# Kernel optimization log

Measured on AMD Instinct MI355X. Metric: run time of the kernel, lower is better.

The kernel has to match this reference:

```python
import jax, jax.numpy as jnp
import numpy as np

B, S, E, H, WIN = 1, 2048, 1024, 16, 256
D = E // H  # head_out = 64


def setup_inputs() -> dict:
    key = jax.random.key(0)
    ks = jax.random.split(key, 10)
    w = lambda k: jax.random.normal(k, (E, E), jnp.float32) * 0.02
    return {
        'x': jax.random.normal(ks[0], (B, S, E), jnp.float32),
        'global_attention_mask': jax.random.randint(ks[1], (B, S), 0, 2).astype(jnp.int32),
        'W_local_query': w(ks[2]),
        'W_local_key': w(ks[3]),
        'W_local_value': w(ks[4]),
        'W_query': w(ks[5]),
        'W_key': w(ks[6]),
        'W_value': w(ks[7]),
        'W_proj': w(ks[8]),
        'b_proj': jnp.zeros((E,), jnp.float32),
    }


def reference(x, global_attention_mask, W_local_query, W_local_key, W_local_value,
              W_query, W_key, W_value, W_proj, b_proj):
    b, seq, emb = x.shape
    nH, dh, win = H, D, WIN
    chunks = seq // win
    NEG = -1e9
    scale = 1.0 / (dh ** 0.5)

    # ---- local (windowed) branch ----
    ql = x @ W_local_query            # [b,S,E]
    kl = x @ W_local_key
    vl = x @ W_local_value
    # NOTE: original does a direct .view -> plain reshape (no head transpose)
    qc = ql.reshape(b, nH, chunks, win, dh)
    kc = kl.reshape(b, nH, chunks, win, dh)
    vloc = vl.reshape(b, nH, seq, dh)
    s = jnp.einsum('bhcqd,bhckd->bhcqk', qc, kc)      # [b,H,C,W,W]
    causal_w = jnp.tril(jnp.ones((win, win), bool))
    s = jnp.where(causal_w, s, NEG) * scale           # mask then /sqrt(d), as in source
    s = s.mean(axis=2)                                # mean over chunks -> [b,H,W,W]
    s = jnp.pad(s, ((0, 0), (0, 0), (0, seq - win), (0, seq - win)))
    aw_l = jax.nn.softmax(s, axis=-1)                 # [b,H,S,S]
    local_ctx = jnp.einsum('bhqk,bhkd->bqhd', aw_l, vloc).reshape(b, seq, emb)

    # ---- global (full) branch ----
    q = (x @ W_query).reshape(b, seq, nH, dh).transpose(0, 2, 1, 3)
    k = (x @ W_key).reshape(b, seq, nH, dh).transpose(0, 2, 1, 3)
    v = (x @ W_value).reshape(b, seq, nH, dh).transpose(0, 2, 1, 3)
    sg = jnp.einsum('bhqd,bhkd->bhqk', q, k)          # [b,H,S,S]
    causal_s = jnp.tril(jnp.ones((seq, seq), bool))
    sg = jnp.where(causal_s, sg, NEG) * scale
    aw_g = jax.nn.softmax(sg, axis=-1)
    gctx = jnp.einsum('bhqk,bhkd->bqhd', aw_g, v).reshape(b, seq, emb)

    # ---- combine via global mask, then output projection ----
    ctx = jnp.where(global_attention_mask[:, :, None] == 1, gctx, local_ctx)
    return ctx @ W_proj + b_proj
```

## Files before the change

### kernel.cpp

```cpp
#include <hip/hip_runtime.h>
#include <hip/hip_bf16.h>

typedef _Float16 h8 __attribute__((ext_vector_type(8)));
typedef _Float16 h4 __attribute__((ext_vector_type(4)));
typedef _Float16 h2 __attribute__((ext_vector_type(2)));
typedef __fp16 fp16x2 __attribute__((ext_vector_type(2)));
typedef float f4 __attribute__((ext_vector_type(4)));

#define S_LEN 2048
#define EMB 1024
#define NH 16
#define DH 64

__device__ __forceinline__ void async_copy16(const void* g, void* l) {
  __builtin_amdgcn_global_load_lds(
      (const __attribute__((address_space(1))) void*)g,
      (__attribute__((address_space(3))) void*)l, 16, 0, 0);
}

__device__ __forceinline__ f4 mfma16(h8 a, h8 b, f4 c) {
  return __builtin_amdgcn_mfma_f32_16x16x32_f16(a, b, c, 0, 0, 0);
}

__device__ __forceinline__ h2 cvt_pk(float a, float b) {
  const fp16x2 r = __builtin_amdgcn_cvt_pkrtz(a, b);
  return __builtin_bit_cast(h2, r);
}

__global__ __launch_bounds__(256) void prep_kernel(
    const float* __restrict__ x, const float* w0, const float* w1, const float* w2,
    const float* w3, const float* w4, const float* w5, const float* w6,
    _Float16* __restrict__ xh, _Float16* __restrict__ Wtb) {
  const int bid = blockIdx.x;
  if (bid < 2048) {
    const int i = bid * 256 + threadIdx.x;
    const float4 v = *(const float4*)&x[(long)i * 4];
    h4 o;
    o.x = (_Float16)v.x; o.y = (_Float16)v.y; o.z = (_Float16)v.z; o.w = (_Float16)v.w;
    *(h4*)&xh[(long)i * 4] = o;
    return;
  }
  const int b2 = bid - 2048;
  const int z = b2 >> 10, rem = b2 & 1023;
  const float* W = w0;
  switch (z) {
    case 1: W = w1; break; case 2: W = w2; break; case 3: W = w3; break;
    case 4: W = w4; break; case 5: W = w5; break; case 6: W = w6; break;
    default: break;
  }
  __shared__ float t[32][33];
  const int bk = (rem & 31) * 32, bn = (rem >> 5) * 32;
  const int tx = threadIdx.x & 31, ty = threadIdx.x >> 5;
  #pragma unroll
  for (int i = 0; i < 4; ++i)
    t[ty + i * 8][tx] = W[(long)(bk + ty + i * 8) * 1024 + bn + tx];
  __syncthreads();
  _Float16* o = Wtb + (long)z * 1048576;
  #pragma unroll
  for (int i = 0; i < 4; ++i)
    o[(long)(bn + ty + i * 8) * 1024 + bk + tx] = (_Float16)t[tx][ty + i * 8];
}

__global__ __launch_bounds__(256) void shuffle_kernel(
    const _Float16* __restrict__ ql, const _Float16* __restrict__ kl,
    const _Float16* __restrict__ vl, const _Float16* __restrict__ vg,
    const int* __restrict__ gmask,
    _Float16* __restrict__ Aq, _Float16* __restrict__ Ak,
    _Float16* __restrict__ vgT, float* __restrict__ Vall, float* __restrict__ Vtail,
    int* __restrict__ qsel, int* __restrict__ qcnt) {
  const int bid = blockIdx.x;
  if (bid < 2048) {
    const _Float16* src = (bid >= 1024) ? kl : ql;
    _Float16* dst = (bid >= 1024) ? Ak : Aq;
    const int u = (bid & 1023) * 256 + threadIdx.x;
    const int dseg = u & 7, c = (u >> 3) & 7, q = (u >> 6) & 255, h = u >> 14;
    const long soff = (long)(h * 128 + c * 16 + (q >> 4)) * 1024 + (q & 15) * 64 + dseg * 8;
    *(h8*)&dst[(long)u * 8] = *(const h8*)&src[soff];
    return;
  }
  if (bid < 4096) {
    const int b2 = bid - 2048;
    __shared__ _Float16 t[32][33];
    const int bs = (b2 & 63) * 32, be = (b2 >> 6) * 32;
    const int tx = threadIdx.x & 31, ty = threadIdx.x >> 5;
    #pragma unroll
    for (int i = 0; i < 4; ++i)
      t[ty + i * 8][tx] = vg[(long)(bs + ty + i * 8) * 1024 + be + tx];
    __syncthreads();
    #pragma unroll
    for (int i = 0; i < 4; ++i)
      vgT[(long)(be + ty + i * 8) * 2048 + bs + tx] = t[tx][ty + i * 8];
    return;
  }
  if (bid < 4112) {
    const int hh = bid - 4096;
    const int d = threadIdx.x & 63, g = threadIdx.x >> 6;
    float sall = 0.f, shead = 0.f;
    for (int i = 0; i < 32; ++i) {
      const int ro = g * 32 + i;
      const _Float16* base = vl + (long)(hh * 128 + ro) * 1024 + d;
      #pragma unroll
      for (int j = 0; j < 16; ++j) {
        const float v = (float)base[j * 64];
        sall += v;
        if (ro < 16) shead += v;
      }
    }
    __shared__ float sA[4][64], sH[4][64];
    sA[g][d] = sall; sH[g][d] = shead;
    __syncthreads();
    if (g == 0) {
      const float a = sA[0][d] + sA[1][d] + sA[2][d] + sA[3][d];
      const float hsum = sH[0][d] + sH[1][d] + sH[2][d] + sH[3][d];
      Vall[hh * 64 + d] = a;
      Vtail[hh * 64 + d] = a - hsum;
    }
    return;
  }
  const int t = threadIdx.x;
  int m8[8], cnt8 = 0;
  #pragma unroll
  for (int j = 0; j < 8; ++j) {
    m8[j] = gmask[t * 8 + j];
    cnt8 += (m8[j] == 1);
  }
  __shared__ int sc[256];
  sc[t] = cnt8;
  __syncthreads();
  for (int off = 1; off < 256; off <<= 1) {
    const int v = (t >= off) ? sc[t - off] : 0;
    __syncthreads();
    sc[t] += v;
    __syncthreads();
  }
  int base = sc[t] - cnt8;
  #pragma unroll
  for (int j = 0; j < 8; ++j)
    if (m8[j] == 1) qsel[base++] = t * 8 + j;
  if (t == 255) qcnt[0] = sc[255];
}


template <bool F32OUT, bool HAS_BIAS, bool REMAP>
__global__ __launch_bounds__(256) void gemm_kernel(
    const _Float16* __restrict__ A, const _Float16* __restrict__ Bt,
    void* __restrict__ Cv, const float* __restrict__ bias,
    int M, int N, int K, long sA, long sB, long sC) {
  int bxx, byy, bzz;
  if constexpr (REMAP) {
    const int bid = blockIdx.x;
    bzz = bid >> 7;
    const int r = bid & 127;
    byy = r & 7;
    bxx = r >> 3;
  } else {
    bxx = blockIdx.x; byy = blockIdx.y; bzz = blockIdx.z;
  }
  const _Float16* Ab = A + (long)bzz * sA;
  const _Float16* Bb = Bt + (long)bzz * sB;
  const int bm = bxx * 128, bn = byy * 128;
  __shared__ alignas(16) _Float16 As[128 * 64];
  __shared__ alignas(16) _Float16 Bs[128 * 64];
  const int tid = threadIdx.x;
  const int w = tid >> 6, l = tid & 63;
  const int lo = l & 15, hi = l >> 4;
  const int wr = (w >> 1) * 64, wc = (w & 1) * 64;
  const int srow = l >> 3, ssp = l & 7;
  const int ssl = ssp ^ (srow & 7);

  const f4 zero = {0.f, 0.f, 0.f, 0.f};
  f4 acc[4][4];
  #pragma unroll
  for (int m = 0; m < 4; ++m)
    #pragma unroll
    for (int n = 0; n < 4; ++n) acc[m][n] = zero;

  for (int k0 = 0; k0 < K; k0 += 64) {
    #pragma unroll
    for (int i = 0; i < 4; ++i) {
      const int chunk = w + i * 4;
      async_copy16(&Ab[(long)(bm + chunk * 8 + srow) * K + k0 + ssl * 8], &As[chunk * 512]);
      async_copy16(&Bb[(long)(bn + chunk * 8 + srow) * K + k0 + ssl * 8], &Bs[chunk * 512]);
    }
    __syncthreads();
    #pragma unroll
    for (int kk = 0; kk < 2; ++kk) {
      h8 af[4], bf[4];
      #pragma unroll
      for (int m = 0; m < 4; ++m) {
        const int r = wr + m * 16 + lo;
        af[m] = *(const h8*)&As[r * 64 + (((kk * 4 + hi) ^ (r & 7)) * 8)];
      }
      #pragma unroll
      for (int n = 0; n < 4; ++n) {
        const int r = wc + n * 16 + lo;
        bf[n] = *(const h8*)&Bs[r * 64 + (((kk * 4 + hi) ^ (r & 7)) * 8)];
      }
      #pragma unroll
      for (int m = 0; m < 4; ++m)
        #pragma unroll
        for (int n = 0; n < 4; ++n)
          acc[m][n] = mfma16(af[m], bf[n], acc[m][n]);
    }
    __syncthreads();
  }

  #pragma unroll
  for (int m = 0; m < 4; ++m) {
    const int row0 = bm + wr + m * 16 + hi * 4;
    #pragma unroll
    for (int n = 0; n < 4; ++n) {
      const int col = bn + wc + n * 16 + lo;
      float bv = 0.f;
      if constexpr (HAS_BIAS) bv = bias[col];
      #pragma unroll
      for (int r = 0; r < 4; ++r) {
        const float v = acc[m][n][r] + bv;
        const long off = (long)bzz * sC + (long)(row0 + r) * N + col;
        if constexpr (F32OUT) ((float*)Cv)[off] = v;
        else ((_Float16*)Cv)[off] = (_Float16)v;
      }
    }
  }
}

__global__ __launch_bounds__(256) void gemm64_kernel(
    const _Float16* __restrict__ A, const _Float16* __restrict__ Bt,
    float* __restrict__ C, const float* __restrict__ bias, int N, int K) {
  const int bm = blockIdx.x * 64, bn = blockIdx.y * 128;
  __shared__ alignas(16) _Float16 As[64 * 64];
  __shared__ alignas(16) _Float16 Bs[128 * 64];
  const int tid = threadIdx.x;
  const int w = tid >> 6, l = tid & 63;
  const int lo = l & 15, hi = l >> 4;
  const int wc = w * 32;
  const int srow = l >> 3, ssp = l & 7;
  const int ssl = ssp ^ (srow & 7);

  const f4 zero = {0.f, 0.f, 0.f, 0.f};
  f4 acc[4][2];
  #pragma unroll
  for (int m = 0; m < 4; ++m)
    #pragma unroll
    for (int n = 0; n < 2; ++n) acc[m][n] = zero;

  for (int k0 = 0; k0 < K; k0 += 64) {
    #pragma unroll
    for (int i = 0; i < 6; ++i) {
      const int c = w + i * 4;
      if (c < 8)
        async_copy16(&A[(long)(bm + c * 8 + srow) * K + k0 + ssl * 8], &As[c * 512]);
      else
        async_copy16(&Bt[(long)(bn + (c - 8) * 8 + srow) * K + k0 + ssl * 8], &Bs[(c - 8) * 512]);
    }
    __syncthreads();
    #pragma unroll
    for (int kk = 0; kk < 2; ++kk) {
      h8 af[4], bf[2];
      #pragma unroll
      for (int m = 0; m < 4; ++m) {
        const int r = m * 16 + lo;
        af[m] = *(const h8*)&As[r * 64 + (((kk * 4 + hi) ^ (r & 7)) * 8)];
      }
      #pragma unroll
      for (int n = 0; n < 2; ++n) {
        const int r = wc + n * 16 + lo;
        bf[n] = *(const h8*)&Bs[r * 64 + (((kk * 4 + hi) ^ (r & 7)) * 8)];
      }
      #pragma unroll
      for (int m = 0; m < 4; ++m)
        #pragma unroll
        for (int n = 0; n < 2; ++n)
          acc[m][n] = mfma16(af[m], bf[n], acc[m][n]);
    }
    __syncthreads();
  }

  #pragma unroll
  for (int m = 0; m < 4; ++m) {
    const int row0 = bm + m * 16 + hi * 4;
    #pragma unroll
    for (int n = 0; n < 2; ++n) {
      const int col = bn + wc + n * 16 + lo;
      const float bv = bias ? bias[col] : 0.f;
      #pragma unroll
      for (int r = 0; r < 4; ++r)
        C[(long)(row0 + r) * N + col] = acc[m][n][r] + bv;
    }
  }
}

__global__ __launch_bounds__(256) void flash_kernel(
    const _Float16* __restrict__ Q, const _Float16* __restrict__ Km,
    const _Float16* __restrict__ Vt, const int* __restrict__ qsel,
    const int* __restrict__ qcnt, _Float16* __restrict__ ctx,
    _Float16* __restrict__ pO, float2* __restrict__ ml) {
  const int bx = blockIdx.x;
  const int h = bx & 15;
  const int v = bx >> 4;
  const int tile = 31 - (v >> 1);
  const int chunk = v & 1;
  const int cnt = qcnt[0];
  if (tile * 64 >= cnt) return;
  const int L = qsel[min(tile * 64 + 63, cnt - 1)] + 1;
  const int ntot = (L + 63) >> 6;
  const bool chunked = (ntot > 16);
  if (!chunked && chunk) return;
  const int nsplit = chunked ? ((ntot + 1) >> 1) : ntot;
  const int t0 = chunk ? nsplit : 0;
  const int t1 = chunk ? ntot : nsplit;

  const int tid = threadIdx.x;
  const int w = tid >> 6, l = tid & 63;
  const int lo = l & 15, hi = l >> 4;
  const int row = tile * 64 + w * 16 + lo;
  const int qg = qsel[min(row, cnt - 1)];

  __shared__ alignas(16) _Float16 Ks[2][64 * 64];
  __shared__ alignas(16) _Float16 Vs[2][64 * 64];
  __shared__ alignas(16) _Float16 Ps[4][16 * 80];
  _Float16* ps = Ps[w];

  const int rl = tid >> 3;
  const int ssl = (tid & 7) ^ (rl & 7);

#define STAGE(b, t)                                                                   \
  do {                                                                                \
    async_copy16(&Km[(long)((t) * 64 + rl) * EMB + h * DH + ssl * 8],                 \
                 &Ks[(b)][(w * 8) * 64]);                                             \
    async_copy16(&Km[(long)((t) * 64 + 32 + rl) * EMB + h * DH + ssl * 8],            \
                 &Ks[(b)][(w * 8 + 32) * 64]);                                        \
    async_copy16(&Vt[(long)(h * DH + rl) * S_LEN + (t) * 64 + ssl * 8],               \
                 &Vs[(b)][(w * 8) * 64]);                                             \
    async_copy16(&Vt[(long)(h * DH + 32 + rl) * S_LEN + (t) * 64 + ssl * 8],          \
                 &Vs[(b)][(w * 8 + 32) * 64]);                                        \
  } while (0)

  h8 qf[2];
  #pragma unroll
  for (int kk = 0; kk < 2; ++kk)
    qf[kk] = *(const h8*)&Q[(long)qg * EMB + h * DH + kk * 32 + hi * 8];

  const f4 zero = {0.f, 0.f, 0.f, 0.f};
  f4 o[4];
  #pragma unroll
  for (int nd = 0; nd < 4; ++nd) o[nd] = zero;
  float mr = -1e30f, lr = 0.f;
  const float SC = 0.125f * 1.44269504f;

  STAGE(0, t0);
  __syncthreads();
  int cur = 0;

  for (int t = t0; t < t1; ++t) {
    if (t + 1 < t1) STAGE(cur ^ 1, t + 1);

    const _Float16* ks = Ks[cur];
    const _Float16* vs = Vs[cur];

    __builtin_amdgcn_s_setprio(1);
    f4 s[4];
    #pragma unroll
    for (int n = 0; n < 4; ++n) {
      s[n] = zero;
      #pragma unroll
      for (int kk = 0; kk < 2; ++kk) {
        const int r = n * 16 + lo;
        const h8 kf = *(const h8*)&ks[r * 64 + (((kk * 4 + hi) ^ (lo & 7)) * 8)];
        s[n] = mfma16(kf, qf[kk], s[n]);
      }
    }
    __builtin_amdgcn_s_setprio(0);

    float sv[16];
    float tm = -1e30f;
    #pragma unroll
    for (int n = 0; n < 4; ++n)
      #pragma unroll
      for (int r = 0; r < 4; ++r) {
        float vv = s[n][r] * SC;
        if ((t * 64 + n * 16 + hi * 4 + r) > qg) vv = -1e30f;
        sv[n * 4 + r] = vv;
        tm = fmaxf(tm, vv);
      }
    tm = fmaxf(tm, __shfl_xor(tm, 16));
    tm = fmaxf(tm, __shfl_xor(tm, 32));
    const float mn = fmaxf(mr, tm);
    const float c = exp2f(mr - mn);
    mr = mn;
    float psum = 0.f;
    #pragma unroll
    for (int i = 0; i < 16; ++i) {
      sv[i] = exp2f(sv[i] - mr);
      psum += sv[i];
    }
    psum += __shfl_xor(psum, 16);
    psum += __shfl_xor(psum, 32);
    lr = lr * c + psum;

    #pragma unroll
    for (int n = 0; n < 4; ++n) {
      const int seg = (2 * n + (hi >> 1)) ^ (lo & 7);
      const int base = lo * 80 + seg * 8 + (hi & 1) * 4;
      *(h2*)&ps[base] = cvt_pk(sv[n * 4 + 0], sv[n * 4 + 1]);
      *(h2*)&ps[base + 2] = cvt_pk(sv[n * 4 + 2], sv[n * 4 + 3]);
    }
    h8 pb[2];
    #pragma unroll
    for (int kk = 0; kk < 2; ++kk)
      pb[kk] = *(const h8*)&ps[lo * 80 + (((kk * 4 + hi) ^ (lo & 7)) * 8)];

    __builtin_amdgcn_s_setprio(1);
    #pragma unroll
    for (int nd = 0; nd < 4; ++nd) {
      #pragma unroll
      for (int r = 0; r < 4; ++r) o[nd][r] *= c;
      #pragma unroll
      for (int kk = 0; kk < 2; ++kk) {
        const int rr = nd * 16 + lo;
        const h8 vf = *(const h8*)&vs[rr * 64 + (((kk * 4 + hi) ^ (lo & 7)) * 8)];
        o[nd] = mfma16(vf, pb[kk], o[nd]);
      }
    }
    __builtin_amdgcn_s_setprio(0);

    __syncthreads();
    cur ^= 1;
  }
#undef STAGE

  if (chunked) {
    const int slot = (h * 32 + tile) * 2 + chunk;
    _Float16* po = pO + (long)slot * 4096 + (w * 16 + lo) * 64;
    #pragma unroll
    for (int nd = 0; nd < 4; ++nd) {
      const h2 a = cvt_pk(o[nd][0], o[nd][1]);
      const h2 b = cvt_pk(o[nd][2], o[nd][3]);
      const h4 v4 = {a[0], a[1], b[0], b[1]};
      *(h4*)&po[nd * 16 + hi * 4] = v4;
    }
    if (hi == 0) ml[slot * 64 + w * 16 + lo] = make_float2(mr, lr);
  } else if (row < cnt) {
    const float inv = 1.f / lr;
    #pragma unroll
    for (int nd = 0; nd < 4; ++nd) {
      const h2 a = cvt_pk(o[nd][0] * inv, o[nd][1] * inv);
      const h2 b = cvt_pk(o[nd][2] * inv, o[nd][3] * inv);
      const h4 v4 = {a[0], a[1], b[0], b[1]};
      *(h4*)&ctx[(long)qg * EMB + h * DH + nd * 16 + hi * 4] = v4;
    }
  }
}

__global__ __launch_bounds__(256) void localfin_kernel(
    const _Float16* __restrict__ P, const _Float16* __restrict__ vl,
    const float* __restrict__ Vall, const float* __restrict__ Vtail,
    const _Float16* __restrict__ pO, const float2* __restrict__ ml,
    const int* __restrict__ gmask, const int* __restrict__ qsel,
    const int* __restrict__ qcnt, _Float16* __restrict__ ctx) {
  const int bid = blockIdx.x;
  const int tid = threadIdx.x;
  if (bid < 1024) {
    const int q = bid & 255, hg = bid >> 8;
    if (gmask[q] == 1) return;
    const int sub = tid >> 6, l = tid & 63;
    const int hh = hg * 4 + sub;
    __shared__ float wgt[4][256];
    const _Float16* Pr = P + ((long)hh * 256 + q) * 256;
    float sv[4];
    bool valid[4];
    float M = -1e30f;
    #pragma unroll
    for (int i = 0; i < 4; ++i) {
      const int k = l + i * 64;
      valid[i] = (k <= q);
      sv[i] = valid[i] ? (float)Pr[k] * 0.015625f : -1e30f;
      M = fmaxf(M, sv[i]);
    }
    M = fmaxf(M, __shfl_xor(M, 1));
    M = fmaxf(M, __shfl_xor(M, 2));
    M = fmaxf(M, __shfl_xor(M, 4));
    M = fmaxf(M, __shfl_xor(M, 8));
    M = fmaxf(M, __shfl_xor(M, 16));
    M = fmaxf(M, __shfl_xor(M, 32));
    M = fmaxf(M, 0.f);
    float ps = 0.f;
    #pragma unroll
    for (int i = 0; i < 4; ++i) {
      const float e = valid[i] ? __expf(sv[i] - M) : 0.f;
      wgt[sub][l + i * 64] = e;
      ps += e;
    }
    ps += __shfl_xor(ps, 1);
    ps += __shfl_xor(ps, 2);
    ps += __shfl_xor(ps, 4);
    ps += __shfl_xor(ps, 8);
    ps += __shfl_xor(ps, 16);
    ps += __shfl_xor(ps, 32);
    const float em = __expf(-M);
    const float denom = ps + 1792.f * em;
    const int d = l;
    float acc = em * Vtail[hh * 64 + d];
    const _Float16* vb = vl + (long)hh * 128 * 1024 + d;
    for (int k = 0; k <= q; ++k)
      acc += wgt[sub][k] * (float)vb[(long)(k >> 4) * 1024 + (k & 15) * 64];
    ctx[(long)q * EMB + hh * DH + d] = (_Float16)(acc / denom);
    return;
  }
  if (bid < 8192) {
    const int gid = (bid - 1024) * 256 + tid;
    const int s = 256 + (gid >> 10), e = gid & 1023;
    if (gmask[s] == 0)
      ctx[(long)s * EMB + e] = (_Float16)(Vall[e] * (1.f / 2048.f));
    return;
  }
  const int b2 = bid - 8192;
  const int h = b2 & 15, tile = b2 >> 4;
  const int cnt = qcnt[0];
  if (tile * 64 >= cnt) return;
  const int L = qsel[min(tile * 64 + 63, cnt - 1)] + 1;
  if (((L + 63) >> 6) <= 16) return;
  const int q = tid >> 2, ds = (tid & 3) * 16;
  const int row = tile * 64 + q;
  if (row >= cnt) return;
  const int sg = qsel[row];
  const int slot0 = (h * 32 + tile) * 2, slot1 = slot0 + 1;
  const float2 ml0 = ml[slot0 * 64 + q];
  const float2 ml1 = ml[slot1 * 64 + q];
  const float M = fmaxf(ml0.x, ml1.x);
  const float w0 = exp2f(ml0.x - M), w1 = exp2f(ml1.x - M);
  const float inv = 1.f / (w0 * ml0.y + w1 * ml1.y);
  const h8 a0 = *(const h8*)&pO[(long)slot0 * 4096 + q * 64 + ds];
  const h8 a1 = *(const h8*)&pO[(long)slot0 * 4096 + q * 64 + ds + 8];
  const h8 b0 = *(const h8*)&pO[(long)slot1 * 4096 + q * 64 + ds];
  const h8 b1 = *(const h8*)&pO[(long)slot1 * 4096 + q * 64 + ds + 8];
  h8 r0, r1;
  #pragma unroll
  for (int j = 0; j < 8; ++j) {
    r0[j] = (_Float16)((w0 * (float)a0[j] + w1 * (float)b0[j]) * inv);
    r1[j] = (_Float16)((w0 * (float)a1[j] + w1 * (float)b1[j]) * inv);
  }
  *(h8*)&ctx[(long)sg * EMB + h * DH + ds] = r0;
  *(h8*)&ctx[(long)sg * EMB + h * DH + ds + 8] = r1;
}

extern "C" void kernel_launch(void* const* d_in, const int* in_sizes, int n_in,
                              void* d_out, int out_size, void* d_ws, size_t ws_size,
                              hipStream_t stream) {
  const float* x = (const float*)d_in[0];
  const int* gmask = (const int*)d_in[1];
  const float* Wlq = (const float*)d_in[2];
  const float* Wlk = (const float*)d_in[3];
  const float* Wlv = (const float*)d_in[4];
  const float* Wq = (const float*)d_in[5];
  const float* Wk = (const float*)d_in[6];
  const float* Wv = (const float*)d_in[7];
  const float* Wp = (const float*)d_in[8];
  const float* bp = (const float*)d_in[9];
  float* out = (float*)d_out;

  char* ws = (char*)d_ws;
  _Float16* xh = (_Float16*)(ws);
  _Float16* Wtb = (_Float16*)(ws + (4u << 20));
  _Float16* proj = (_Float16*)(ws + (18u << 20));
  _Float16* ql = proj;
  _Float16* kl = (_Float16*)(ws + (22u << 20));
  _Float16* vl = (_Float16*)(ws + (26u << 20));
  _Float16* qg = (_Float16*)(ws + (30u << 20));
  _Float16* kg = (_Float16*)(ws + (34u << 20));
  _Float16* vg = (_Float16*)(ws + (38u << 20));
  _Float16* Aq = (_Float16*)(ws + (4u << 20));
  _Float16* Ak = (_Float16*)(ws + (8u << 20));
  _Float16* P = (_Float16*)(ws + (12u << 20));
  float* Vall = (float*)(ws + (14u << 20));
  float* Vtail = (float*)(ws + (14u << 20) + 4096);
  float2* ml = (float2*)(ws + (14u << 20) + 16384);
  int* qsel = (int*)(ws + (14u << 20) + 614400);
  int* qcnt = (int*)(ws + (14u << 20) + 622592);
  _Float16* Wpt = (_Float16*)(ws + (16u << 20));
  _Float16* vgT = (_Float16*)(ws);
  _Float16* ctx = (_Float16*)(ws + (18u << 20));
  _Float16* pO = (_Float16*)(ws + (4u << 20));

  prep_kernel<<<9216, 256, 0, stream>>>(x, Wlq, Wlk, Wlv, Wq, Wk, Wv, Wp, xh, Wtb);
  gemm_kernel<false, false, true><<<768, 256, 0, stream>>>(
      xh, Wtb, proj, nullptr, 2048, 1024, 1024, 0L, 1048576L, 2097152L);
  shuffle_kernel<<<4113, 256, 0, stream>>>(ql, kl, vl, vg, gmask, Aq, Ak, vgT,
                                           Vall, Vtail, qsel, qcnt);
  gemm_kernel<false, false, false><<<dim3(2, 2, 16), 256, 0, stream>>>(
      Aq, Ak, P, nullptr, 256, 256, 512, 131072L, 131072L, 65536L);
  flash_kernel<<<1024, 256, 0, stream>>>(qg, kg, vgT, qsel, qcnt, ctx, pO, ml);
  localfin_kernel<<<8704, 256, 0, stream>>>(P, vl, Vall, Vtail, pO, ml, gmask,
                                            qsel, qcnt, ctx);
  gemm64_kernel<<<dim3(32, 8), 256, 0, stream>>>(ctx, Wpt, out, bp, 1024, 1024);
}
```

Baseline: 141.2 us.

## Replace QKV projection GEMM with 256x256-tile double-buffered pipelined kernel

The fused six-way input projection GEMM (2048x6144x1024) now runs in a new 512-thread kernel. Each block computes a 256x256 tile with double-buffered async global-to-LDS loads, interleaves loads with MFMA phases, raises wave priority around the MFMAs, and uses 192 blocks instead of 768 128x128 blocks. The aim is more data reuse per block and load latency hidden behind compute. The flash and combine kernels also clamp qcnt and mask qsel indices, a defensive guard against out-of-range values. The risk is a heavier register and LDS footprint, which lowers occupancy, and a single partial wave of blocks.

```diff
diff --git a/kernel.cpp b/kernel.cpp
--- a/kernel.cpp
+++ b/kernel.cpp
@@ -140,22 +140,124 @@
   if (t == 255) qcnt[0] = sc[255];
 }
 
-
-template <bool F32OUT, bool HAS_BIAS, bool REMAP>
+__global__ __launch_bounds__(512, 2) void gemm256_kernel(
+    const _Float16* __restrict__ A, const _Float16* __restrict__ Bt,
+    _Float16* __restrict__ C) {
+  const int bid = blockIdx.x;
+  const int bxx = (bid >> 3) & 7;
+  const int byy = (bid & 7) * 3 + (bid >> 6);
+  const int bm = bxx * 256, bn = byy * 256;
+
+  __shared__ alignas(16) _Float16 As[2][2][8192];
+  __shared__ alignas(16) _Float16 Bs[2][2][8192];
+
+  const int tid = threadIdx.x;
+  const int w = tid >> 6, l = tid & 63;
+  const int lo = l & 15, hi = l >> 4;
+  const int wm = w >> 2, wn = w & 3;
+  const int srow = tid >> 3;
+  const int kseg = (tid & 7) ^ (srow & 7);
+
+  const _Float16* Bb = Bt + (long)(byy >> 2) * 1048576 + (long)(bn & 1023) * 1024;
+
+#define STG_A(db, half, tt) do {                                                     \
+    const int t_ = (tt) < 15 ? (tt) : 15;                                            \
+    const _Float16* s_ = A + (long)(bm + (half) * 128 + srow) * 1024 + t_ * 64 + kseg * 8; \
+    async_copy16(s_, &As[db][half][w * 512]);                                        \
+    async_copy16(s_ + 65536, &As[db][half][4096 + w * 512]);                         \
+  } while (0)
+#define STG_B(db, half, tt) do {                                                     \
+    const int t_ = (tt) < 15 ? (tt) : 15;                                            \
+    const _Float16* s_ = Bb + (long)((half) * 128 + srow) * 1024 + t_ * 64 + kseg * 8; \
+    async_copy16(s_, &Bs[db][half][w * 512]);                                        \
+    async_copy16(s_ + 65536, &Bs[db][half][4096 + w * 512]);                         \
+  } while (0)
+#define LDA(db, mg) do { _Pragma("unroll")                                           \
+    for (int fr = 0; fr < 4; ++fr) {                                                 \
+      const int rr = wm * 64 + fr * 16 + lo;                                         \
+      _Pragma("unroll") for (int kk = 0; kk < 2; ++kk)                               \
+        af[fr][kk] = *(const h8*)&As[db][mg][rr * 64 + (((kk * 4 + hi) ^ (rr & 7)) * 8)]; \
+    } } while (0)
+#define LDB(db, ng) do { _Pragma("unroll")                                           \
+    for (int fc = 0; fc < 2; ++fc) {                                                 \
+      const int rr = wn * 32 + fc * 16 + lo;                                         \
+      _Pragma("unroll") for (int kk = 0; kk < 2; ++kk)                               \
+        bf[ng][fc][kk] = *(const h8*)&Bs[db][ng][rr * 64 + (((kk * 4 + hi) ^ (rr & 7)) * 8)]; \
+    } } while (0)
+#define MFMA_PH(mg, ng) do {                                                         \
+    __builtin_amdgcn_s_setprio(1);                                                   \
+    _Pragma("unroll") for (int fr = 0; fr < 4; ++fr)                                 \
+      _Pragma("unroll") for (int fc = 0; fc < 2; ++fc) {                             \
+        acc[mg][fr][ng][fc] = mfma16(af[fr][0], bf[ng][fc][0], acc[mg][fr][ng][fc]); \
+        acc[mg][fr][ng][fc] = mfma16(af[fr][1], bf[ng][fc][1], acc[mg][fr][ng][fc]); \
+      }                                                                              \
+    __builtin_amdgcn_s_setprio(0);                                                   \
+  } while (0)
+#define BARR do { asm volatile("" ::: "memory"); __builtin_amdgcn_s_barrier();       \
+                  asm volatile("" ::: "memory"); } while (0)
+#define VM8 asm volatile("s_waitcnt vmcnt(8)" ::: "memory")
+
+  const f4 zero = {0.f, 0.f, 0.f, 0.f};
+  f4 acc[2][4][2][2];
+  #pragma unroll
+  for (int a_ = 0; a_ < 2; ++a_)
+    #pragma unroll
+    for (int b_ = 0; b_ < 4; ++b_)
+      #pragma unroll
+      for (int c_ = 0; c_ < 2; ++c_)
+        #pragma unroll
+        for (int d_ = 0; d_ < 2; ++d_) acc[a_][b_][c_][d_] = zero;
+  h8 af[4][2];
+  h8 bf[2][2][2];
+
+  STG_A(0, 0, 0); STG_B(0, 0, 0); STG_A(0, 1, 0); STG_B(0, 1, 0);
+  STG_A(1, 0, 1); STG_B(1, 0, 1); STG_A(1, 1, 1);
+  asm volatile("s_waitcnt vmcnt(6)" ::: "memory");
+  BARR;
+
+  for (int i = 0; i < 8; ++i) {
+    const int t2 = 2 * i + 2, t3 = 2 * i + 3;
+    LDA(0, 0); LDB(0, 0); STG_B(1, 1, 2 * i + 1); MFMA_PH(0, 0); VM8; BARR;
+    LDB(0, 1); STG_A(0, 0, t2); MFMA_PH(0, 1); BARR;
+    LDA(0, 1); STG_B(0, 0, t2); MFMA_PH(1, 0); BARR;
+    STG_A(0, 1, t2); MFMA_PH(1, 1); VM8; BARR;
+    LDA(1, 0); LDB(1, 0); STG_B(0, 1, t2); MFMA_PH(0, 0); VM8; BARR;
+    LDB(1, 1); STG_A(1, 0, t3); MFMA_PH(0, 1); BARR;
+    LDA(1, 1); STG_B(1, 0, t3); MFMA_PH(1, 0); BARR;
+    STG_A(1, 1, t3); MFMA_PH(1, 1); VM8; BARR;
+  }
+
+  #pragma unroll
+  for (int mg = 0; mg < 2; ++mg)
+    #pragma unroll
+    for (int fr = 0; fr < 4; ++fr) {
+      const int row = bm + mg * 128 + wm * 64 + fr * 16 + hi * 4;
+      #pragma unroll
+      for (int ng = 0; ng < 2; ++ng)
+        #pragma unroll
+        for (int fc = 0; fc < 2; ++fc) {
+          const int colg = bn + ng * 128 + wn * 32 + fc * 16 + lo;
+          _Float16* cp = C + (long)(colg >> 10) * 2097152 + (long)row * 1024 + (colg & 1023);
+          #pragma unroll
+          for (int r = 0; r < 4; ++r)
+            cp[(long)r * 1024] = (_Float16)acc[mg][fr][ng][fc][r];
+        }
+    }
+#undef STG_A
+#undef STG_B
+#undef LDA
+#undef LDB
+#undef MFMA_PH
+#undef BARR
+#undef VM8
+}
+
+template <bool F32OUT, bool HAS_BIAS>
 __global__ __launch_bounds__(256) void gemm_kernel(
     const _Float16* __restrict__ A, const _Float16* __restrict__ Bt,
     void* __restrict__ Cv, const float* __restrict__ bias,
     int M, int N, int K, long sA, long sB, long sC) {
-  int bxx, byy, bzz;
-  if constexpr (REMAP) {
-    const int bid = blockIdx.x;
-    bzz = bid >> 7;
-    const int r = bid & 127;
-    byy = r & 7;
-    bxx = r >> 3;
-  } else {
-    bxx = blockIdx.x; byy = blockIdx.y; bzz = blockIdx.z;
-  }
+  const int bxx = blockIdx.x, byy = blockIdx.y, bzz = blockIdx.z;
   const _Float16* Ab = A + (long)bzz * sA;
   const _Float16* Bb = Bt + (long)bzz * sB;
   const int bm = bxx * 128, bn = byy * 128;
@@ -185,7 +287,7 @@
     __syncthreads();
     #pragma unroll
     for (int kk = 0; kk < 2; ++kk) {
-      h8 af[4], bf[4];
+      h8 af[4], bff[4];
       #pragma unroll
       for (int m = 0; m < 4; ++m) {
         const int r = wr + m * 16 + lo;
@@ -194,13 +296,13 @@
       #pragma unroll
       for (int n = 0; n < 4; ++n) {
         const int r = wc + n * 16 + lo;
-        bf[n] = *(const h8*)&Bs[r * 64 + (((kk * 4 + hi) ^ (r & 7)) * 8)];
+        bff[n] = *(const h8*)&Bs[r * 64 + (((kk * 4 + hi) ^ (r & 7)) * 8)];
       }
       #pragma unroll
       for (int m = 0; m < 4; ++m)
         #pragma unroll
         for (int n = 0; n < 4; ++n)
-          acc[m][n] = mfma16(af[m], bf[n], acc[m][n]);
+          acc[m][n] = mfma16(af[m], bff[n], acc[m][n]);
     }
     __syncthreads();
   }
@@ -256,7 +358,7 @@
     __syncthreads();
     #pragma unroll
     for (int kk = 0; kk < 2; ++kk) {
-      h8 af[4], bf[2];
+      h8 af[4], bff[2];
       #pragma unroll
       for (int m = 0; m < 4; ++m) {
         const int r = m * 16 + lo;
@@ -265,13 +367,13 @@
       #pragma unroll
       for (int n = 0; n < 2; ++n) {
         const int r = wc + n * 16 + lo;
-        bf[n] = *(const h8*)&Bs[r * 64 + (((kk * 4 + hi) ^ (r & 7)) * 8)];
+        bff[n] = *(const h8*)&Bs[r * 64 + (((kk * 4 + hi) ^ (r & 7)) * 8)];
       }
       #pragma unroll
       for (int m = 0; m < 4; ++m)
         #pragma unroll
         for (int n = 0; n < 2; ++n)
-          acc[m][n] = mfma16(af[m], bf[n], acc[m][n]);
+          acc[m][n] = mfma16(af[m], bff[n], acc[m][n]);
     }
     __syncthreads();
   }
@@ -300,9 +402,10 @@
   const int v = bx >> 4;
   const int tile = 31 - (v >> 1);
   const int chunk = v & 1;
-  const int cnt = qcnt[0];
+  int cnt = qcnt[0];
+  cnt = cnt < 1 ? 1 : (cnt > 2048 ? 2048 : cnt);
   if (tile * 64 >= cnt) return;
-  const int L = qsel[min(tile * 64 + 63, cnt - 1)] + 1;
+  const int L = (qsel[min(tile * 64 + 63, cnt - 1)] & 2047) + 1;
   const int ntot = (L + 63) >> 6;
   const bool chunked = (ntot > 16);
   if (!chunked && chunk) return;
@@ -314,7 +417,7 @@
   const int w = tid >> 6, l = tid & 63;
   const int lo = l & 15, hi = l >> 4;
   const int row = tile * 64 + w * 16 + lo;
-  const int qg = qsel[min(row, cnt - 1)];
+  const int qg = qsel[min(row, cnt - 1)] & 2047;
 
   __shared__ alignas(16) _Float16 Ks[2][64 * 64];
   __shared__ alignas(16) _Float16 Vs[2][64 * 64];
@@ -516,14 +619,15 @@
   }
   const int b2 = bid - 8192;
   const int h = b2 & 15, tile = b2 >> 4;
-  const int cnt = qcnt[0];
+  int cnt = qcnt[0];
+  cnt = cnt < 1 ? 1 : (cnt > 2048 ? 2048 : cnt);
   if (tile * 64 >= cnt) return;
-  const int L = qsel[min(tile * 64 + 63, cnt - 1)] + 1;
+  const int L = (qsel[min(tile * 64 + 63, cnt - 1)] & 2047) + 1;
   if (((L + 63) >> 6) <= 16) return;
   const int q = tid >> 2, ds = (tid & 3) * 16;
   const int row = tile * 64 + q;
   if (row >= cnt) return;
-  const int sg = qsel[row];
+  const int sg = qsel[row] & 2047;
   const int slot0 = (h * 32 + tile) * 2, slot1 = slot0 + 1;
   const float2 ml0 = ml[slot0 * 64 + q];
   const float2 ml1 = ml[slot1 * 64 + q];
@@ -583,11 +687,10 @@
   _Float16* pO = (_Float16*)(ws + (4u << 20));
 
   prep_kernel<<<9216, 256, 0, stream>>>(x, Wlq, Wlk, Wlv, Wq, Wk, Wv, Wp, xh, Wtb);
-  gemm_kernel<false, false, true><<<768, 256, 0, stream>>>(
-      xh, Wtb, proj, nullptr, 2048, 1024, 1024, 0L, 1048576L, 2097152L);
+  gemm256_kernel<<<192, 512, 0, stream>>>(xh, Wtb, proj);
   shuffle_kernel<<<4113, 256, 0, stream>>>(ql, kl, vl, vg, gmask, Aq, Ak, vgT,
                                            Vall, Vtail, qsel, qcnt);
-  gemm_kernel<false, false, false><<<dim3(2, 2, 16), 256, 0, stream>>>(
+  gemm_kernel<false, false><<<dim3(2, 2, 16), 256, 0, stream>>>(
       Aq, Ak, P, nullptr, 256, 256, 512, 131072L, 131072L, 65536L);
   flash_kernel<<<1024, 256, 0, stream>>>(qg, kg, vgT, qsel, qcnt, ctx, pO, ml);
   localfin_kernel<<<8704, 256, 0, stream>>>(P, vl, Vall, Vtail, pO, ml, gmask,
```

Measured after the change: 140.1 us. Within noise of the previous version (-0.8%).
